# Optimization experiments

Measured on AMD Instinct MI355X. Metric: run time of the kernel, lower is better.

## Reference

```python
import jax, jax.numpy as jnp
import numpy as np
from jax import lax

B, C, D, H, W = 2, 64, 20, 20, 20


def _conv3d(x, w, b, pad):
    # x: [B,C,D,H,W], w: [O,I,kd,kh,kw]
    y = lax.conv_general_dilated(
        x, w, window_strides=(1, 1, 1), padding=pad,
        dimension_numbers=('NCDHW', 'OIDHW', 'NCDHW'))
    return y + b[None, :, None, None, None]


def setup_inputs() -> dict:
    key = jax.random.key(0)
    ks = jax.random.split(key, 7)
    s = 1.0 / np.sqrt(C * 3)  # conv fan-in = C*1*3*1
    return {
        'x': jax.random.normal(ks[0], (B, C, D, H, W), jnp.float32),
        'q_w': jax.random.uniform(ks[1], (C, C, 1, 3, 1), jnp.float32, -s, s),
        'q_b': jax.random.uniform(ks[2], (C,), jnp.float32, -s, s),
        'k_w': jax.random.uniform(ks[3], (C, C, 3, 1, 1), jnp.float32, -s, s),
        'k_b': jax.random.uniform(ks[4], (C,), jnp.float32, -s, s),
        'v_w': jax.random.uniform(ks[5], (C, C, 1, 1, 3), jnp.float32, -s, s),
        'v_b': jax.random.uniform(ks[6], (C,), jnp.float32, -s, s),
    }


def reference(x, q_w, q_b, k_w, k_b, v_w, v_b):
    b, c, d, h, w = x.shape
    n = d * h * w
    q0 = _conv3d(x, q_w, q_b, ((0, 0), (1, 1), (0, 0))).reshape(b, c, n)
    k0 = _conv3d(x, k_w, k_b, ((1, 1), (0, 0), (0, 0))).reshape(b, c, n)
    v = _conv3d(x, v_w, v_b, ((0, 0), (0, 0), (1, 1))).reshape(b, c, n)
    # scores[b, i, j] = sum_c k0[b,c,i] * q0[b,c,j]  -> [B, N, N]
    scores = jnp.einsum('bci,bcj->bij', k0, q0)
    # torch Softmax(dim=1) on [B,N,N] normalizes over axis 1 (the i axis)
    attn = jax.nn.softmax(scores, axis=1)
    out = jnp.einsum('bcn,bnm->bcm', v, attn)  # v @ attn
    return out.reshape(b, c, d, h, w)
```

## Files before the change

kernel.cpp:

```cpp
#include <hip/hip_runtime.h>
#include <cstdint>
#include <cstddef>

typedef _Float16 half4_t  __attribute__((ext_vector_type(4)));
typedef _Float16 half8_t  __attribute__((ext_vector_type(8)));
typedef short    short4_t __attribute__((ext_vector_type(4)));
typedef unsigned short ushort4_t __attribute__((ext_vector_type(4)));
typedef float    f32x4_t  __attribute__((ext_vector_type(4)));

#define LOG2E 1.44269504088896340736f

__device__ __forceinline__ float bf2f(unsigned short u) {
    union { unsigned int u; float f; } x;
    x.u = ((unsigned int)u) << 16;
    return x.f;
}
__device__ __forceinline__ unsigned short f2bf(float f) {
    union { float f; unsigned int u; } x;
    x.f = f;
    unsigned int r = (x.u + 0x7FFFu + ((x.u >> 16) & 1u)) >> 16;
    return (unsigned short)r;
}
__device__ __forceinline__ unsigned short f2bf_fast(float f) {
    union { float f; unsigned int u; } x;
    x.f = f;
    return (unsigned short)((x.u + 0x8000u) >> 16);
}

__global__ __launch_bounds__(256) void prep_kernel(
    const void* __restrict__ x,
    const void* __restrict__ qw, const void* __restrict__ kw, const void* __restrict__ vw,
    const void* __restrict__ qb, const void* __restrict__ kb, const void* __restrict__ vb,
    int* __restrict__ flag,
    _Float16* __restrict__ w2, float* __restrict__ bb, _Float16* __restrict__ xT)
{
    __shared__ int scnt;
    __shared__ _Float16 tile[64][66];

    if (threadIdx.x == 0) scnt = 0;
    __syncthreads();
    {
        unsigned int w = ((const unsigned int*)x)[threadIdx.x];
        int e = (w >> 7) & 0xFF;
        int hit = (e == 0) || (e >= 0x68 && e <= 0x88);
        atomicAdd(&scnt, hit);
    }
    __syncthreads();
    const int bf = (scnt >= 128) ? 1 : 0;
    if (blockIdx.x == 0 && threadIdx.x == 0) flag[0] = bf;

    if (blockIdx.x < 144) {
        int idx = blockIdx.x * 256 + threadIdx.x;
        if (idx < 36864) {
            int conv = idx / 12288;
            int r    = idx - conv * 12288;
            int tap  = r >> 12;
            int r2   = r & 4095;
            int co   = r2 >> 6;
            int ci   = r2 & 63;
            const void* w = (conv == 0) ? qw : (conv == 1) ? kw : vw;
            float t;
            if (bf) t = bf2f(((const unsigned short*)w)[co * 192 + ci * 3 + tap]);
            else    t = ((const float*)w)[co * 192 + ci * 3 + tap];
            if (conv == 0) t *= LOG2E;
            w2[idx] = (_Float16)t;
        }
        if (idx < 192) {
            int a = idx >> 6, co = idx & 63;
            const void* s = (a == 0) ? qb : (a == 1) ? kb : vb;
            float t = bf ? bf2f(((const unsigned short*)s)[co]) : ((const float*)s)[co];
            if (a == 0) t *= LOG2E;
            bb[idx] = t;
        }
    } else {
        const int bx   = blockIdx.x - 144;
        const int b    = bx / 125;
        const int n0   = (bx - b * 125) * 64;
        const int lane = threadIdx.x & 63;
        const int wv   = threadIdx.x >> 6;

        if (bf) {
            const unsigned short* xb = (const unsigned short*)x + (size_t)b * 512000 + n0 + lane;
#pragma unroll
            for (int i = 0; i < 16; ++i) {
                const int ci = wv * 16 + i;
                tile[ci][lane] = (_Float16)bf2f(xb[(size_t)ci * 8000]);
            }
        } else {
            const float* xb = (const float*)x + (size_t)b * 512000 + n0 + lane;
#pragma unroll
            for (int i = 0; i < 16; ++i) {
                const int ci = wv * 16 + i;
                tile[ci][lane] = (_Float16)xb[(size_t)ci * 8000];
            }
        }
        __syncthreads();
        _Float16* out = xT + ((size_t)b * 8000 + n0) * 64 + lane;
#pragma unroll
        for (int i = 0; i < 16; ++i) {
            const int r = wv * 16 + i;
            out[(size_t)r * 64] = tile[lane][r];
        }
    }
}

__global__ __launch_bounds__(256, 2) void convg_kernel(
    const _Float16* __restrict__ xT, const _Float16* __restrict__ w2,
    const float* __restrict__ bb,
    _Float16* __restrict__ Qt, _Float16* __restrict__ Kt, unsigned short* __restrict__ Vt)
{
    const int tid = threadIdx.x;
    const int wv  = tid >> 6;
    const int L   = tid & 63;
    const int q4  = L >> 4;
    const int lm  = L & 15;
    const int W    = blockIdx.x * 4 + wv;
    const int conv = W % 3;
    const int u    = W / 3;
    const int b    = u / 250;
    const int n0   = (u - b * 250) * 32;

    half8_t wf[3][2][4];
    const _Float16* wbase = w2 + (size_t)conv * 12288;
#pragma unroll
    for (int tap = 0; tap < 3; ++tap)
#pragma unroll
        for (int kh = 0; kh < 2; ++kh)
#pragma unroll
            for (int cb = 0; cb < 4; ++cb)
                wf[tap][kh][cb] = *(const half8_t*)(
                    wbase + ((size_t)(tap * 64 + cb * 16 + lm)) * 64 + kh * 32 + q4 * 8);

    f32x4_t acc[2][4];
#pragma unroll
    for (int cb = 0; cb < 4; ++cb) {
        const float bi = bb[conv * 64 + cb * 16 + lm];
        const f32x4_t v = (f32x4_t){bi, bi, bi, bi};
        acc[0][cb] = v;
        acc[1][cb] = v;
    }

    const _Float16* xb = xT + (size_t)b * 512000;
    const half8_t z8 = {(_Float16)0, (_Float16)0, (_Float16)0, (_Float16)0,
                        (_Float16)0, (_Float16)0, (_Float16)0, (_Float16)0};

#pragma unroll
    for (int mt = 0; mt < 2; ++mt) {
        const int npos = n0 + mt * 16 + lm;
        int gm, gp, off;
        if (conv == 0)      { const int h = (npos / 20) % 20; gm = h > 0; gp = h < 19; off = 20; }
        else if (conv == 1) { const int d = npos / 400;       gm = d > 0; gp = d < 19; off = 400; }
        else                { const int w = npos % 20;        gm = w > 0; gp = w < 19; off = 1; }
        const int rm = gm ? npos - off : npos;
        const int rp = gp ? npos + off : npos;

#pragma unroll
        for (int kh = 0; kh < 2; ++kh) {
            const int ko = kh * 32 + q4 * 8;
            half8_t a0 = *(const half8_t*)(xb + (size_t)rm * 64 + ko);
            const half8_t a1 = *(const half8_t*)(xb + (size_t)npos * 64 + ko);
            half8_t a2 = *(const half8_t*)(xb + (size_t)rp * 64 + ko);
            a0 = gm ? a0 : z8;
            a2 = gp ? a2 : z8;
#pragma unroll
            for (int cb = 0; cb < 4; ++cb) {
                acc[mt][cb] = __builtin_amdgcn_mfma_f32_16x16x32_f16(a0, wf[0][kh][cb], acc[mt][cb], 0, 0, 0);
                acc[mt][cb] = __builtin_amdgcn_mfma_f32_16x16x32_f16(a1, wf[1][kh][cb], acc[mt][cb], 0, 0, 0);
                acc[mt][cb] = __builtin_amdgcn_mfma_f32_16x16x32_f16(a2, wf[2][kh][cb], acc[mt][cb], 0, 0, 0);
            }
        }
    }

    if (conv < 2) {
        _Float16* dst = (conv == 0) ? Qt : Kt;
#pragma unroll
        for (int mt = 0; mt < 2; ++mt)
#pragma unroll
            for (int cb = 0; cb < 4; ++cb)
#pragma unroll
                for (int reg = 0; reg < 4; ++reg) {
                    const int n = n0 + mt * 16 + q4 * 4 + reg;
                    dst[((size_t)b * 8000 + n) * 64 + cb * 16 + lm] = (_Float16)acc[mt][cb][reg];
                }
    } else {
#pragma unroll
        for (int mt = 0; mt < 2; ++mt)
#pragma unroll
            for (int cb = 0; cb < 4; ++cb) {
                ushort4_t vvv;
#pragma unroll
                for (int reg = 0; reg < 4; ++reg) vvv[reg] = f2bf(acc[mt][cb][reg]);
                *(ushort4_t*)(Vt + ((size_t)b * 64 + cb * 16 + lm) * 8000 + n0 + mt * 16 + q4 * 4) = vvv;
            }
    }
}

__global__ __launch_bounds__(256, 2) void attn_kernel(
    const _Float16* __restrict__ Qt, const _Float16* __restrict__ Kt,
    const unsigned short* __restrict__ Vt,
    _Float16* __restrict__ Oseg, float* __restrict__ Wseg)
{
    __shared__ __align__(16) _Float16       k_lds[2][4096];
    __shared__ __align__(16) unsigned short v_lds[2][4096];

    const int tid = threadIdx.x;
    const int wv  = tid >> 6;
    const int L   = tid & 63;
    const int q4  = L >> 4;
    const int lm  = L & 15;
    const int qt  = blockIdx.x;
    const int b   = blockIdx.y;
    const int sp  = blockIdx.z;
    const int NS  = gridDim.z;
    const int t0  = (125 * sp) / NS;
    const int t1  = (125 * (sp + 1)) / NS;
    const int unit = qt * 4 + wv;

    const _Float16* Qb = Qt + ((size_t)b * 8000 + (size_t)qt * 128 + wv * 32 + lm) * 64 + q4 * 8;
    half8_t bq00 = *(const half8_t*)(Qb);
    half8_t bq01 = *(const half8_t*)(Qb + 32);
    half8_t bq10 = *(const half8_t*)(Qb + 16 * 64);
    half8_t bq11 = *(const half8_t*)(Qb + 16 * 64 + 32);

    f32x4_t o[2][4];
    f32x4_t acc_l[2];
#pragma unroll
    for (int mt = 0; mt < 2; ++mt) {
        acc_l[mt] = (f32x4_t){0.f, 0.f, 0.f, 0.f};
#pragma unroll
        for (int cb = 0; cb < 4; ++cb) o[mt][cb] = (f32x4_t){0.f, 0.f, 0.f, 0.f};
    }
    const short4_t ones4 = {(short)0x3F80, (short)0x3F80, (short)0x3F80, (short)0x3F80};

    const _Float16*       Kg = Kt + (size_t)b * 512000;
    const unsigned short* Vg = Vt + (size_t)b * 512000;
    const int r0  = tid >> 3;
    const int cc0 = tid & 7;
    const int swz_lo = r0 * 64 + ((cc0 ^ (r0 & 7)) * 8);
    const int swz_hi = (r0 + 32) * 64 + ((cc0 ^ (r0 & 7)) * 8);
    const _Float16*       Kr0 = Kg + (size_t)r0 * 64 + cc0 * 8;
    const _Float16*       Kr1 = Kg + (size_t)(r0 + 32) * 64 + cc0 * 8;
    const unsigned short* Vr0 = Vg + (size_t)r0 * 8000 + cc0 * 8;
    const unsigned short* Vr1 = Vg + (size_t)(r0 + 32) * 8000 + cc0 * 8;

    uint4 sk0, sk1, sv0, sv1;

    {
        const int n0 = t0 * 64;
        sk0 = *(const uint4*)(Kr0 + (size_t)n0 * 64);
        sk1 = *(const uint4*)(Kr1 + (size_t)n0 * 64);
        sv0 = *(const uint4*)(Vr0 + n0);
        sv1 = *(const uint4*)(Vr1 + n0);
        *(uint4*)(&k_lds[0][swz_lo]) = sk0;
        *(uint4*)(&k_lds[0][swz_hi]) = sk1;
        *(uint4*)(&v_lds[0][swz_lo]) = sv0;
        *(uint4*)(&v_lds[0][swz_hi]) = sv1;
        if (t0 + 1 < t1) {
            const int n1 = (t0 + 1) * 64;
            sk0 = *(const uint4*)(Kr0 + (size_t)n1 * 64);
            sk1 = *(const uint4*)(Kr1 + (size_t)n1 * 64);
            sv0 = *(const uint4*)(Vr0 + n1);
            sv1 = *(const uint4*)(Vr1 + n1);
        }
    }

    int p = 0;
    for (int kt = t0; kt < t1; ++kt) {
        __syncthreads();
        if (kt + 1 < t1) {
            *(uint4*)(&k_lds[p ^ 1][swz_lo]) = sk0;
            *(uint4*)(&k_lds[p ^ 1][swz_hi]) = sk1;
            *(uint4*)(&v_lds[p ^ 1][swz_lo]) = sv0;
            *(uint4*)(&v_lds[p ^ 1][swz_hi]) = sv1;
            if (kt + 2 < t1) {
                const int n2 = (kt + 2) * 64;
                sk0 = *(const uint4*)(Kr0 + (size_t)n2 * 64);
                sk1 = *(const uint4*)(Kr1 + (size_t)n2 * 64);
                sv0 = *(const uint4*)(Vr0 + n2);
                sv1 = *(const uint4*)(Vr1 + n2);
            }
        }

        short4_t pfr[2][4];
#pragma unroll
        for (int ns = 0; ns < 4; ++ns) {
            const int n = ns * 16 + lm;
            const _Float16* krow = &k_lds[p][n * 64];
            const half8_t ak0 = *(const half8_t*)(krow + (((q4    ) ^ (n & 7)) * 8));
            const half8_t ak1 = *(const half8_t*)(krow + (((q4 + 4) ^ (n & 7)) * 8));
#pragma unroll
            for (int mt = 0; mt < 2; ++mt) {
                f32x4_t z = (f32x4_t){0.f, 0.f, 0.f, 0.f};
                z = __builtin_amdgcn_mfma_f32_16x16x32_f16(ak0, mt ? bq10 : bq00, z, 0, 0, 0);
                z = __builtin_amdgcn_mfma_f32_16x16x32_f16(ak1, mt ? bq11 : bq01, z, 0, 0, 0);
                short4_t pk;
#pragma unroll
                for (int reg = 0; reg < 4; ++reg)
                    pk[reg] = (short)f2bf_fast(exp2f(z[reg]));
                pfr[mt][ns] = pk;
            }
        }

#pragma unroll
        for (int mt = 0; mt < 2; ++mt)
#pragma unroll
            for (int ns = 0; ns < 4; ++ns)
                acc_l[mt] = __builtin_amdgcn_mfma_f32_16x16x16bf16_1k(ones4, pfr[mt][ns], acc_l[mt], 0, 0, 0);

#pragma unroll
        for (int cb = 0; cb < 4; ++cb) {
            const int c = cb * 16 + lm;
            const unsigned short* vrow = &v_lds[p][c * 64];
            f32x4_t a0 = o[0][cb], a1 = o[1][cb];
#pragma unroll
            for (int ns = 0; ns < 4; ++ns) {
                const int cc = ns * 2 + (q4 >> 1);
                const short4_t av = *(const short4_t*)(vrow + ((cc ^ (c & 7)) * 8) + (q4 & 1) * 4);
                a0 = __builtin_amdgcn_mfma_f32_16x16x16bf16_1k(av, pfr[0][ns], a0, 0, 0, 0);
                a1 = __builtin_amdgcn_mfma_f32_16x16x16bf16_1k(av, pfr[1][ns], a1, 0, 0, 0);
            }
            o[0][cb] = a0;
            o[1][cb] = a1;
        }
        p ^= 1;
    }

    if (unit >= 250) return;

    float rinv[2], lg[2];
#pragma unroll
    for (int mt = 0; mt < 2; ++mt) {
        const float l = acc_l[mt][0];
        rinv[mt] = 1.0f / l;
        lg[mt]   = __log2f(l);
    }

    const int seg = (b * 250 + unit) * NS + sp;
    _Float16* os = Oseg + (size_t)seg * 2048;
#pragma unroll
    for (int mt = 0; mt < 2; ++mt) {
#pragma unroll
        for (int cb = 0; cb < 4; ++cb) {
            half4_t e;
#pragma unroll
            for (int reg = 0; reg < 4; ++reg) e[reg] = (_Float16)(o[mt][cb][reg] * rinv[mt]);
            *(half4_t*)(os + (mt * 16 + lm) * 64 + cb * 16 + q4 * 4) = e;
        }
    }
    if (q4 == 0) {
#pragma unroll
        for (int mt = 0; mt < 2; ++mt)
            Wseg[(size_t)seg * 32 + mt * 16 + lm] = lg[mt];
    }
}

__global__ __launch_bounds__(256, 2) void combine_kernel(
    const _Float16* __restrict__ Oseg, const float* __restrict__ Wseg,
    const int* __restrict__ flag, void* __restrict__ outv, int NS)
{
    __shared__ float wls[16 * 32];
    __shared__ float cls[16 * 32];
    const int tid = threadIdx.x;
    const int qt = blockIdx.x, b = blockIdx.y;
    const int base = (b * 250 + qt) * NS;

    for (int i = tid; i < NS * 32; i += 256) wls[i] = Wseg[(size_t)base * 32 + i];
    __syncthreads();
    if (tid < 32) {
        const int r = tid;
        float wm = wls[r];
        for (int s2 = 1; s2 < NS; ++s2) wm = fmaxf(wm, wls[s2 * 32 + r]);
        float cs = 0.f;
        for (int s2 = 0; s2 < NS; ++s2) {
            float cc = exp2f(wls[s2 * 32 + r] - wm);
            cls[s2 * 32 + r] = cc;
            cs += cc;
        }
        const float inv = 1.f / cs;
        for (int s2 = 0; s2 < NS; ++s2) cls[s2 * 32 + r] *= inv;
    }
    __syncthreads();

    const int c = tid & 63, rg = tid >> 6;
    float acc[8];
#pragma unroll
    for (int i = 0; i < 8; ++i) acc[i] = 0.f;
    for (int s2 = 0; s2 < NS; ++s2) {
        const _Float16* src = Oseg + ((size_t)(base + s2)) * 2048 + rg * 8 * 64 + c;
        const float* cf = &cls[s2 * 32 + rg * 8];
#pragma unroll
        for (int i = 0; i < 8; ++i) acc[i] += (float)src[i * 64] * cf[i];
    }

    const size_t ob = ((size_t)b * 64 + c) * 8000 + qt * 32 + rg * 8;
    if (*flag) {
        uint4 u0;
        u0.x = f2bf(acc[0]) | ((unsigned)f2bf(acc[1]) << 16);
        u0.y = f2bf(acc[2]) | ((unsigned)f2bf(acc[3]) << 16);
        u0.z = f2bf(acc[4]) | ((unsigned)f2bf(acc[5]) << 16);
        u0.w = f2bf(acc[6]) | ((unsigned)f2bf(acc[7]) << 16);
        *(uint4*)((unsigned short*)outv + ob) = u0;
    } else {
        float* o32 = (float*)outv + ob;
        *(f32x4_t*)(o32)     = (f32x4_t){acc[0], acc[1], acc[2], acc[3]};
        *(f32x4_t*)(o32 + 4) = (f32x4_t){acc[4], acc[5], acc[6], acc[7]};
    }
}

extern "C" void kernel_launch(void* const* d_in, const int* in_sizes, int n_in,
                              void* d_out, int out_size, void* d_ws, size_t ws_size,
                              hipStream_t stream)
{
    (void)in_sizes; (void)n_in; (void)out_size;
    const void* x  = d_in[0];
    const void* qw = d_in[1];
    const void* qb = d_in[2];
    const void* kw = d_in[3];
    const void* kb = d_in[4];
    const void* vw = d_in[5];
    const void* vb = d_in[6];

    char* ws = (char*)d_ws;
    int*            flag = (int*)ws;
    float*          bb   = (float*)(ws + 2304);
    _Float16*       w2   = (_Float16*)(ws + 3072);
    _Float16*       Qt   = (_Float16*)(ws + 76800);
    _Float16*       Kt   = (_Float16*)(ws + 2124800);
    unsigned short* Vt   = (unsigned short*)(ws + 4172800);
    _Float16*       xT   = (_Float16*)(ws + 6220800);

    const size_t need16 = 6220800 + (size_t)2 * 250 * 16 * 2048 * 2 + (size_t)2 * 250 * 16 * 32 * 4;
    const size_t need8  = 6220800 + (size_t)2 * 250 * 8  * 2048 * 2 + (size_t)2 * 250 * 8  * 32 * 4;
    const int NS = (ws_size >= need16) ? 16 : (ws_size >= need8) ? 8 : 1;
    _Float16* Oseg = (_Float16*)(ws + 6220800);
    float*    Wseg = (float*)(ws + 6220800 + (size_t)2 * 250 * NS * 2048 * 2);

    prep_kernel<<<dim3(394), 256, 0, stream>>>(x, qw, kw, vw, qb, kb, vb, flag, w2, bb, xT);
    convg_kernel<<<dim3(375), 256, 0, stream>>>(xT, w2, bb, Qt, Kt, Vt);
    attn_kernel<<<dim3(63, 2, NS), 256, 0, stream>>>(Qt, Kt, Vt, Oseg, Wseg);
    combine_kernel<<<dim3(250, 2), 256, 0, stream>>>(Oseg, Wseg, flag, d_out, NS);
}
```

Measured before the change: 154.1 us.

## Use single-buffered LDS tiles and truncating bf16 conversion in attention loop

```diff
diff --git a/kernel.cpp b/kernel.cpp
--- a/kernel.cpp
+++ b/kernel.cpp
@@ -21,10 +21,10 @@
     unsigned int r = (x.u + 0x7FFFu + ((x.u >> 16) & 1u)) >> 16;
     return (unsigned short)r;
 }
-__device__ __forceinline__ unsigned short f2bf_fast(float f) {
+__device__ __forceinline__ unsigned short f2bf_trunc(float f) {
     union { float f; unsigned int u; } x;
     x.f = f;
-    return (unsigned short)((x.u + 0x8000u) >> 16);
+    return (unsigned short)(x.u >> 16);
 }
 
 __global__ __launch_bounds__(256) void prep_kernel(
@@ -200,8 +200,8 @@
     const unsigned short* __restrict__ Vt,
     _Float16* __restrict__ Oseg, float* __restrict__ Wseg)
 {
-    __shared__ __align__(16) _Float16       k_lds[2][4096];
-    __shared__ __align__(16) unsigned short v_lds[2][4096];
+    __shared__ __align__(16) _Float16       k_lds[4096];
+    __shared__ __align__(16) unsigned short v_lds[4096];
 
     const int tid = threadIdx.x;
     const int wv  = tid >> 6;
@@ -251,41 +251,28 @@
         sk1 = *(const uint4*)(Kr1 + (size_t)n0 * 64);
         sv0 = *(const uint4*)(Vr0 + n0);
         sv1 = *(const uint4*)(Vr1 + n0);
-        *(uint4*)(&k_lds[0][swz_lo]) = sk0;
-        *(uint4*)(&k_lds[0][swz_hi]) = sk1;
-        *(uint4*)(&v_lds[0][swz_lo]) = sv0;
-        *(uint4*)(&v_lds[0][swz_hi]) = sv1;
-        if (t0 + 1 < t1) {
-            const int n1 = (t0 + 1) * 64;
+    }
+
+    for (int kt = t0; kt < t1; ++kt) {
+        __syncthreads();
+        *(uint4*)(&k_lds[swz_lo]) = sk0;
+        *(uint4*)(&k_lds[swz_hi]) = sk1;
+        *(uint4*)(&v_lds[swz_lo]) = sv0;
+        *(uint4*)(&v_lds[swz_hi]) = sv1;
+        if (kt + 1 < t1) {
+            const int n1 = (kt + 1) * 64;
             sk0 = *(const uint4*)(Kr0 + (size_t)n1 * 64);
             sk1 = *(const uint4*)(Kr1 + (size_t)n1 * 64);
             sv0 = *(const uint4*)(Vr0 + n1);
             sv1 = *(const uint4*)(Vr1 + n1);
         }
-    }
-
-    int p = 0;
-    for (int kt = t0; kt < t1; ++kt) {
         __syncthreads();
-        if (kt + 1 < t1) {
-            *(uint4*)(&k_lds[p ^ 1][swz_lo]) = sk0;
-            *(uint4*)(&k_lds[p ^ 1][swz_hi]) = sk1;
-            *(uint4*)(&v_lds[p ^ 1][swz_lo]) = sv0;
-            *(uint4*)(&v_lds[p ^ 1][swz_hi]) = sv1;
-            if (kt + 2 < t1) {
-                const int n2 = (kt + 2) * 64;
-                sk0 = *(const uint4*)(Kr0 + (size_t)n2 * 64);
-                sk1 = *(const uint4*)(Kr1 + (size_t)n2 * 64);
-                sv0 = *(const uint4*)(Vr0 + n2);
-                sv1 = *(const uint4*)(Vr1 + n2);
-            }
-        }
 
         short4_t pfr[2][4];
 #pragma unroll
         for (int ns = 0; ns < 4; ++ns) {
             const int n = ns * 16 + lm;
-            const _Float16* krow = &k_lds[p][n * 64];
+            const _Float16* krow = &k_lds[n * 64];
             const half8_t ak0 = *(const half8_t*)(krow + (((q4    ) ^ (n & 7)) * 8));
             const half8_t ak1 = *(const half8_t*)(krow + (((q4 + 4) ^ (n & 7)) * 8));
 #pragma unroll
@@ -296,7 +283,7 @@
                 short4_t pk;
 #pragma unroll
                 for (int reg = 0; reg < 4; ++reg)
-                    pk[reg] = (short)f2bf_fast(exp2f(z[reg]));
+                    pk[reg] = (short)f2bf_trunc(exp2f(z[reg]));
                 pfr[mt][ns] = pk;
             }
         }
@@ -310,7 +297,7 @@
 #pragma unroll
         for (int cb = 0; cb < 4; ++cb) {
             const int c = cb * 16 + lm;
-            const unsigned short* vrow = &v_lds[p][c * 64];
+            const unsigned short* vrow = &v_lds[c * 64];
             f32x4_t a0 = o[0][cb], a1 = o[1][cb];
 #pragma unroll
             for (int ns = 0; ns < 4; ++ns) {
@@ -322,7 +309,6 @@
             o[0][cb] = a0;
             o[1][cb] = a1;
         }
-        p ^= 1;
     }
 
     if (unit >= 250) return;
```

Result: slower. 157.5 us (+2.2%).
